# Kernel tuning notes

Measured on AMD Instinct MI355X. Metric: run time of the kernel, lower is better.

The kernel has to match this reference:

```python
import jax, jax.numpy as jnp
import numpy as np

K_NEIGHBORS = 8  # sparse_reads


def setup_inputs() -> dict:
    key = jax.random.key(0)
    k1, k2, k3, k4 = jax.random.split(key, 4)
    b, m, w, r, d_in = 32, 65536, 32, 4, 256
    xi = jax.random.normal(k1, (b, d_in), jnp.float32)
    sparse = jax.random.normal(k2, (b, m, w), jnp.float32)
    W_rk = jax.random.normal(k3, (r * w, d_in), jnp.float32) * 0.05  # read_keys_transform weight
    b_rk = jax.random.normal(k4, (r * w,), jnp.float32) * 0.01       # read_keys_transform bias
    return {"xi": xi, "sparse": sparse, "W_rk": W_rk, "b_rk": b_rk}


def reference(xi, sparse, W_rk, b_rk):
    b = xi.shape[0]
    m, w = sparse.shape[1], sparse.shape[2]
    r = W_rk.shape[0] // w
    # read keys: Linear(input_size, r*w) -> [b, r, w]
    read_keys = (xi @ W_rk.T + b_rk).reshape(b, r, w)
    # exact kNN replacing FLANN: squared L2 distances [b, r, m]
    d2 = (
        jnp.sum(read_keys * read_keys, -1)[..., None]
        - 2.0 * jnp.einsum('brw,bmw->brm', read_keys, sparse)
        + jnp.sum(sparse * sparse, -1)[:, None, :]
    )
    neg_d, idx = jax.lax.top_k(-d2, K_NEIGHBORS)  # K smallest distances
    dist = -neg_d                                  # [b, r, K]
    # gather the K nearest memory rows per (batch, head): [b, r, K, w]
    vecs = sparse[jnp.arange(b)[:, None, None], idx]
    # distances normalized by their max (per key), as in `distances / max(distances)`
    read_weights = dist / jnp.max(dist, -1, keepdims=True)
    # torch code stacks per-key over batch then over keys -> [r, b, K, w]
    read_vectors = jnp.transpose(vecs, (1, 0, 2, 3))
    read_weights = jnp.transpose(read_weights, (1, 0, 2))  # [r, b, K]
    return read_vectors, read_weights
```

## Files before the change

### kernel.cpp

```cpp
#include <hip/hip_runtime.h>

constexpr int Bb = 32;
constexpr int Mm = 65536;
constexpr int Ww = 32;
constexpr int Rr = 4;
constexpr int Dd = 256;
constexpr int Kk = 8;

constexpr int NB_A = 64;
constexpr int TPB_A = 256;
constexpr int ROWS_PER_BLOCK = Mm / NB_A;
constexpr int TILE_ROWS = 128;
constexpr int TILES = ROWS_PER_BLOCK / TILE_ROWS;
constexpr int NBUF = 3;
constexpr int CPL = NB_A * Kk / 64;

__device__ __forceinline__ void glds16(const float4* src, float4* dst_lds) {
  __builtin_amdgcn_global_load_lds(
      (const __attribute__((address_space(1))) void*)src,
      (__attribute__((address_space(3))) void*)dst_lds, 16, 0, 0);
}

__global__ __launch_bounds__(128) void rk_kernel(
    const float* __restrict__ xi, const float* __restrict__ Wrk,
    const float* __restrict__ brk, float* __restrict__ rk,
    float* __restrict__ rknorm) {
  const int b = blockIdx.x;
  const int tid = threadIdx.x;
  __shared__ float xs[Dd];
  __shared__ float rks[Rr * Ww];
  #pragma unroll
  for (int i = 0; i < Dd; i += 128) xs[i + tid] = xi[b * Dd + i + tid];
  __syncthreads();
  float acc = brk[tid];
  const float4* wr = reinterpret_cast<const float4*>(Wrk + (size_t)tid * Dd);
  #pragma unroll 4
  for (int i = 0; i < Dd / 4; ++i) {
    float4 wv = wr[i];
    acc = fmaf(wv.x, xs[4 * i + 0], acc);
    acc = fmaf(wv.y, xs[4 * i + 1], acc);
    acc = fmaf(wv.z, xs[4 * i + 2], acc);
    acc = fmaf(wv.w, xs[4 * i + 3], acc);
  }
  rk[b * Rr * Ww + tid] = acc;
  rks[tid] = acc;
  __syncthreads();
  if (tid < Rr) {
    float s = 0.f;
    #pragma unroll
    for (int j = 0; j < Ww; ++j) s = fmaf(rks[tid * Ww + j], rks[tid * Ww + j], s);
    rknorm[b * Rr + tid] = s;
  }
}

__global__ __launch_bounds__(TPB_A)
__attribute__((amdgpu_waves_per_eu(2, 3)))
void topk_partial(
    const float* __restrict__ sparse, const float* __restrict__ rk,
    const float* __restrict__ rknorm, float* __restrict__ cand_d,
    int* __restrict__ cand_i) {
  const int b = blockIdx.y;
  const int tid = threadIdx.x;
  const int lane = tid & 63;
  const int wid = tid >> 6;
  const float INF = __builtin_inff();

  __shared__ float4 rk4[Rr][8];
  __shared__ float rkn_s[Rr];
  __shared__ float4 tile[NBUF][TILE_ROWS * 8];

  const int rowBlk = blockIdx.x * ROWS_PER_BLOCK;
  const float4* sb4 =
      reinterpret_cast<const float4*>(sparse) + (size_t)b * Mm * 8;
  const int perm = ((lane >> 3) * 8) + ((lane & 7) ^ (lane >> 3));

  auto STAGE = [&](int buf, int t) {
    const float4* g0 = sb4 + (size_t)(rowBlk + t * TILE_ROWS + wid * 32) * 8;
    float4* l0 = &tile[buf][wid * 32 * 8];
    #pragma unroll
    for (int i = 0; i < 4; ++i) glds16(g0 + i * 64 + perm, l0 + i * 64);
  };

  STAGE(0, 0);
  STAGE(1, 1);

  if (tid < Rr * Ww) reinterpret_cast<float*>(rk4)[tid] = rk[b * Rr * Ww + tid];
  if (tid < Rr) rkn_s[tid] = rknorm[b * Rr + tid];
  __syncthreads();

  const int rowL = wid * 32 + (lane >> 1);
  const int rmask = rowL & 7;
  const int hsel = (tid & 1) * 4;

  float4 rkq[Rr][4];
  #pragma unroll
  for (int r = 0; r < Rr; ++r)
    #pragma unroll
    for (int j = 0; j < 4; ++j) rkq[r][j] = rk4[r][hsel + j];

  float d8[Rr][TILES];

  #pragma unroll
  for (int t = 0; t < TILES; ++t) {
    if (t + 2 < TILES) {
      asm volatile("s_waitcnt lgkmcnt(0)" ::: "memory");
      STAGE((t + 2) % NBUF, t + 2);
      asm volatile("s_waitcnt vmcnt(8)" ::: "memory");
    } else if (t + 1 < TILES) {
      asm volatile("s_waitcnt vmcnt(4)" ::: "memory");
    } else {
      asm volatile("s_waitcnt vmcnt(0)" ::: "memory");
    }
    const float4* tb = &tile[t % NBUF][rowL * 8];
    float a0 = 0.f, a1 = 0.f, a2 = 0.f, a3 = 0.f, ss = 0.f;
    #pragma unroll
    for (int j = 0; j < 4; ++j) {
      float4 v = tb[(hsel + j) ^ rmask];
      float4 k0 = rkq[0][j];
      float4 k1 = rkq[1][j];
      float4 k2 = rkq[2][j];
      float4 k3 = rkq[3][j];
      a0 = fmaf(k0.x, v.x, a0); a0 = fmaf(k0.y, v.y, a0);
      a0 = fmaf(k0.z, v.z, a0); a0 = fmaf(k0.w, v.w, a0);
      a1 = fmaf(k1.x, v.x, a1); a1 = fmaf(k1.y, v.y, a1);
      a1 = fmaf(k1.z, v.z, a1); a1 = fmaf(k1.w, v.w, a1);
      a2 = fmaf(k2.x, v.x, a2); a2 = fmaf(k2.y, v.y, a2);
      a2 = fmaf(k2.z, v.z, a2); a2 = fmaf(k2.w, v.w, a2);
      a3 = fmaf(k3.x, v.x, a3); a3 = fmaf(k3.y, v.y, a3);
      a3 = fmaf(k3.z, v.z, a3); a3 = fmaf(k3.w, v.w, a3);
      ss = fmaf(v.x, v.x, ss); ss = fmaf(v.y, v.y, ss);
      ss = fmaf(v.z, v.z, ss); ss = fmaf(v.w, v.w, ss);
    }
    float p0 = fmaf(-2.f, a0, ss);
    float p1 = fmaf(-2.f, a1, ss);
    float p2 = fmaf(-2.f, a2, ss);
    float p3 = fmaf(-2.f, a3, ss);
    p0 += __shfl_xor(p0, 1);
    p1 += __shfl_xor(p1, 1);
    p2 += __shfl_xor(p2, 1);
    p3 += __shfl_xor(p3, 1);
    d8[0][t] = p0;
    d8[1][t] = p1;
    d8[2][t] = p2;
    d8[3][t] = p3;
  }

  __syncthreads();
  float* dmp = reinterpret_cast<float*>(&tile[0][0]);
  if ((tid & 1) == 0) {
    const int e = tid >> 1;
    #pragma unroll
    for (int r = 0; r < Rr; ++r) {
      float4* p = reinterpret_cast<float4*>(&dmp[(r * 128 + e) * 8]);
      p[0] = make_float4(d8[r][0], d8[r][1], d8[r][2], d8[r][3]);
      p[1] = make_float4(d8[r][4], d8[r][5], d8[r][6], d8[r][7]);
    }
  }
  __syncthreads();

  {
    const int r = wid;
    const int e0 = 2 * lane;
    const float rknr = rkn_s[r];
    float v[2][TILES];
    #pragma unroll
    for (int q = 0; q < 2; ++q) {
      const float4* p =
          reinterpret_cast<const float4*>(&dmp[(r * 128 + e0 + q) * 8]);
      float4 lo = p[0], hi = p[1];
      v[q][0] = lo.x; v[q][1] = lo.y; v[q][2] = lo.z; v[q][3] = lo.w;
      v[q][4] = hi.x; v[q][5] = hi.y; v[q][6] = hi.z; v[q][7] = hi.w;
    }
    const int base = rowBlk + e0;
    size_t o = ((size_t)(b * Rr + r) * NB_A + blockIdx.x) * Kk;
    #pragma unroll
    for (int k = 0; k < Kk; ++k) {
      float lv = v[0][0];
      int lrow = base;
      #pragma unroll
      for (int q = 0; q < 2; ++q)
        #pragma unroll
        for (int s = 0; s < TILES; ++s) {
          if (q == 0 && s == 0) continue;
          int row = base + q + s * TILE_ROWS;
          if (v[q][s] < lv || (v[q][s] == lv && row < lrow)) {
            lv = v[q][s]; lrow = row;
          }
        }
      float bv = lv;
      int bi = lrow;
      #pragma unroll
      for (int off = 32; off; off >>= 1) {
        float ov = __shfl_xor(bv, off);
        int oi = __shfl_xor(bi, off);
        if (ov < bv || (ov == bv && oi < bi)) { bv = ov; bi = oi; }
      }
      if (lane == 0) { cand_d[o + k] = bv + rknr; cand_i[o + k] = bi; }
      #pragma unroll
      for (int q = 0; q < 2; ++q)
        #pragma unroll
        for (int s = 0; s < TILES; ++s) {
          bool clr = (v[q][s] == bv) && (base + q + s * TILE_ROWS == bi);
          v[q][s] = clr ? INF : v[q][s];
        }
    }
  }
}

__global__ __launch_bounds__(64) void topk_final(
    const float* __restrict__ sparse, const float* __restrict__ cand_d,
    const int* __restrict__ cand_i, float* __restrict__ out) {
  const int br = blockIdx.x;
  const int b = br >> 2;
  const int r = br & 3;
  const int lane = threadIdx.x;
  const float INF = __builtin_inff();

  float ld[CPL];
  int li[CPL];
  const float* cd = cand_d + (size_t)br * (NB_A * Kk);
  const int* ci = cand_i + (size_t)br * (NB_A * Kk);
  #pragma unroll
  for (int t = 0; t < CPL; ++t) {
    ld[t] = cd[t * 64 + lane];
    li[t] = ci[t * 64 + lane];
  }
  #pragma unroll
  for (int i = 0; i < CPL - 1; ++i)
    #pragma unroll
    for (int j = 0; j < CPL - 1 - i; ++j)
      if (ld[j + 1] < ld[j] || (ld[j + 1] == ld[j] && li[j + 1] < li[j])) {
        float td = ld[j]; ld[j] = ld[j + 1]; ld[j + 1] = td;
        int ti = li[j]; li[j] = li[j + 1]; li[j + 1] = ti;
      }

  __shared__ float s_td[Kk];
  __shared__ int s_ti[Kk];
  #pragma unroll
  for (int k = 0; k < Kk; ++k) {
    float v = ld[0];
    int id = li[0];
    #pragma unroll
    for (int off = 32; off; off >>= 1) {
      float ov = __shfl_xor(v, off);
      int oi = __shfl_xor(id, off);
      if (ov < v || (ov == v && oi < id)) { v = ov; id = oi; }
    }
    if (lane == 0) { s_td[k] = v; s_ti[k] = id; }
    if (li[0] == id) {
      #pragma unroll
      for (int j = 0; j < CPL - 1; ++j) { ld[j] = ld[j + 1]; li[j] = li[j + 1]; }
      ld[CPL - 1] = INF;
      li[CPL - 1] = -1;
    }
  }
  __syncthreads();

  const float dmax = s_td[Kk - 1];
  if (lane < Kk)
    out[(size_t)Rr * Bb * Kk * Ww + ((size_t)r * Bb + b) * Kk + lane] =
        s_td[lane] / dmax;

  const float* sbase = sparse + (size_t)b * Mm * Ww;
  #pragma unroll
  for (int t = 0; t < (Kk * Ww) / 64; ++t) {
    int e = t * 64 + lane;
    int k = e >> 5;
    int j = e & 31;
    out[(((size_t)r * Bb + b) * Kk + k) * Ww + j] =
        sbase[(size_t)s_ti[k] * Ww + j];
  }
}

extern "C" void kernel_launch(void* const* d_in, const int* in_sizes, int n_in,
                              void* d_out, int out_size, void* d_ws,
                              size_t ws_size, hipStream_t stream) {
  const float* xi = (const float*)d_in[0];
  const float* sparse = (const float*)d_in[1];
  const float* Wrk = (const float*)d_in[2];
  const float* brk = (const float*)d_in[3];
  float* out = (float*)d_out;

  char* ws = (char*)d_ws;
  float* rk = (float*)ws;
  float* rknorm = (float*)(ws + 16384);
  float* cand_d = (float*)(ws + 16896);
  int* cand_i = (int*)(ws + 16896 + 262144);

  rk_kernel<<<Bb, 128, 0, stream>>>(xi, Wrk, brk, rk, rknorm);
  dim3 gridA(NB_A, Bb);
  topk_partial<<<gridA, TPB_A, 0, stream>>>(sparse, rk, rknorm, cand_d, cand_i);
  topk_final<<<Bb * Rr, 64, 0, stream>>>(sparse, cand_d, cand_i, out);
}
```

Before: 99.96 us.

## Split topk_partial across twice as many blocks with 4-lane rows and deeper prefetch

Doubles the number of row blocks per batch and halves the tile height, so each row is now handled by 4 lanes instead of 2 and the LDS pipeline is deepened to 4 buffers with 3 tiles in flight. The goal is higher occupancy (waves_per_eu 4) and more memory-level parallelism for the streaming pass over the sparse memory, which is bandwidth bound. The per-block top-k selection is simplified to one value per tile per lane. The cost is twice as many candidates for topk_final to merge and an extra shuffle per row, and the workspace offset for cand_i moves to match.

```diff
diff --git a/kernel.cpp b/kernel.cpp
--- a/kernel.cpp
+++ b/kernel.cpp
@@ -7,12 +7,12 @@
 constexpr int Dd = 256;
 constexpr int Kk = 8;
 
-constexpr int NB_A = 64;
+constexpr int NB_A = 128;
 constexpr int TPB_A = 256;
 constexpr int ROWS_PER_BLOCK = Mm / NB_A;
-constexpr int TILE_ROWS = 128;
+constexpr int TILE_ROWS = 64;
 constexpr int TILES = ROWS_PER_BLOCK / TILE_ROWS;
-constexpr int NBUF = 3;
+constexpr int NBUF = 4;
 constexpr int CPL = NB_A * Kk / 64;
 
 __device__ __forceinline__ void glds16(const float4* src, float4* dst_lds) {
@@ -54,7 +54,7 @@
 }
 
 __global__ __launch_bounds__(TPB_A)
-__attribute__((amdgpu_waves_per_eu(2, 3)))
+__attribute__((amdgpu_waves_per_eu(4)))
 void topk_partial(
     const float* __restrict__ sparse, const float* __restrict__ rk,
     const float* __restrict__ rknorm, float* __restrict__ cand_d,
@@ -69,53 +69,56 @@
   __shared__ float rkn_s[Rr];
   __shared__ float4 tile[NBUF][TILE_ROWS * 8];
 
+  if (tid < Rr * Ww) reinterpret_cast<float*>(rk4)[tid] = rk[b * Rr * Ww + tid];
+  if (tid < Rr) rkn_s[tid] = rknorm[b * Rr + tid];
+  __syncthreads();
+
   const int rowBlk = blockIdx.x * ROWS_PER_BLOCK;
   const float4* sb4 =
       reinterpret_cast<const float4*>(sparse) + (size_t)b * Mm * 8;
   const int perm = ((lane >> 3) * 8) + ((lane & 7) ^ (lane >> 3));
 
+  const int rowL = wid * 16 + (lane >> 2);
+  const int rmask = rowL & 7;
+  const int c0 = 2 * (lane & 3);
+
+  float4 rkq[Rr][2];
+  #pragma unroll
+  for (int r = 0; r < Rr; ++r) {
+    rkq[r][0] = rk4[r][c0];
+    rkq[r][1] = rk4[r][c0 + 1];
+  }
+
+  float d8[Rr][TILES];
+
   auto STAGE = [&](int buf, int t) {
-    const float4* g0 = sb4 + (size_t)(rowBlk + t * TILE_ROWS + wid * 32) * 8;
-    float4* l0 = &tile[buf][wid * 32 * 8];
-    #pragma unroll
-    for (int i = 0; i < 4; ++i) glds16(g0 + i * 64 + perm, l0 + i * 64);
+    const float4* g0 = sb4 + (size_t)(rowBlk + t * TILE_ROWS + wid * 16) * 8;
+    float4* l0 = &tile[buf][wid * 16 * 8];
+    #pragma unroll
+    for (int i = 0; i < 2; ++i) glds16(g0 + i * 64 + perm, l0 + i * 64);
   };
 
   STAGE(0, 0);
   STAGE(1, 1);
-
-  if (tid < Rr * Ww) reinterpret_cast<float*>(rk4)[tid] = rk[b * Rr * Ww + tid];
-  if (tid < Rr) rkn_s[tid] = rknorm[b * Rr + tid];
-  __syncthreads();
-
-  const int rowL = wid * 32 + (lane >> 1);
-  const int rmask = rowL & 7;
-  const int hsel = (tid & 1) * 4;
-
-  float4 rkq[Rr][4];
-  #pragma unroll
-  for (int r = 0; r < Rr; ++r)
-    #pragma unroll
-    for (int j = 0; j < 4; ++j) rkq[r][j] = rk4[r][hsel + j];
-
-  float d8[Rr][TILES];
-
+  STAGE(2, 2);
   #pragma unroll
   for (int t = 0; t < TILES; ++t) {
-    if (t + 2 < TILES) {
+    if (t + 3 < TILES) {
       asm volatile("s_waitcnt lgkmcnt(0)" ::: "memory");
-      STAGE((t + 2) % NBUF, t + 2);
-      asm volatile("s_waitcnt vmcnt(8)" ::: "memory");
+      STAGE((t + 3) % NBUF, t + 3);
+      asm volatile("s_waitcnt vmcnt(6)" ::: "memory");
+    } else if (t + 2 < TILES) {
+      asm volatile("s_waitcnt vmcnt(4)" ::: "memory");
     } else if (t + 1 < TILES) {
-      asm volatile("s_waitcnt vmcnt(4)" ::: "memory");
+      asm volatile("s_waitcnt vmcnt(2)" ::: "memory");
     } else {
       asm volatile("s_waitcnt vmcnt(0)" ::: "memory");
     }
     const float4* tb = &tile[t % NBUF][rowL * 8];
     float a0 = 0.f, a1 = 0.f, a2 = 0.f, a3 = 0.f, ss = 0.f;
     #pragma unroll
-    for (int j = 0; j < 4; ++j) {
-      float4 v = tb[(hsel + j) ^ rmask];
+    for (int j = 0; j < 2; ++j) {
+      float4 v = tb[(c0 + j) ^ rmask];
       float4 k0 = rkq[0][j];
       float4 k1 = rkq[1][j];
       float4 k2 = rkq[2][j];
@@ -135,10 +138,10 @@
     float p1 = fmaf(-2.f, a1, ss);
     float p2 = fmaf(-2.f, a2, ss);
     float p3 = fmaf(-2.f, a3, ss);
-    p0 += __shfl_xor(p0, 1);
-    p1 += __shfl_xor(p1, 1);
-    p2 += __shfl_xor(p2, 1);
-    p3 += __shfl_xor(p3, 1);
+    p0 += __shfl_xor(p0, 1); p0 += __shfl_xor(p0, 2);
+    p1 += __shfl_xor(p1, 1); p1 += __shfl_xor(p1, 2);
+    p2 += __shfl_xor(p2, 1); p2 += __shfl_xor(p2, 2);
+    p3 += __shfl_xor(p3, 1); p3 += __shfl_xor(p3, 2);
     d8[0][t] = p0;
     d8[1][t] = p1;
     d8[2][t] = p2;
@@ -147,46 +150,31 @@
 
   __syncthreads();
   float* dmp = reinterpret_cast<float*>(&tile[0][0]);
-  if ((tid & 1) == 0) {
-    const int e = tid >> 1;
-    #pragma unroll
-    for (int r = 0; r < Rr; ++r) {
-      float4* p = reinterpret_cast<float4*>(&dmp[(r * 128 + e) * 8]);
-      p[0] = make_float4(d8[r][0], d8[r][1], d8[r][2], d8[r][3]);
-      p[1] = make_float4(d8[r][4], d8[r][5], d8[r][6], d8[r][7]);
-    }
+  if ((lane & 3) == 0) {
+    #pragma unroll
+    for (int r = 0; r < Rr; ++r)
+      #pragma unroll
+      for (int t = 0; t < TILES; ++t)
+        dmp[r * ROWS_PER_BLOCK + t * TILE_ROWS + rowL] = d8[r][t];
   }
   __syncthreads();
 
   {
     const int r = wid;
-    const int e0 = 2 * lane;
     const float rknr = rkn_s[r];
-    float v[2][TILES];
-    #pragma unroll
-    for (int q = 0; q < 2; ++q) {
-      const float4* p =
-          reinterpret_cast<const float4*>(&dmp[(r * 128 + e0 + q) * 8]);
-      float4 lo = p[0], hi = p[1];
-      v[q][0] = lo.x; v[q][1] = lo.y; v[q][2] = lo.z; v[q][3] = lo.w;
-      v[q][4] = hi.x; v[q][5] = hi.y; v[q][6] = hi.z; v[q][7] = hi.w;
-    }
-    const int base = rowBlk + e0;
+    float v[TILES];
+    #pragma unroll
+    for (int i = 0; i < TILES; ++i)
+      v[i] = dmp[r * ROWS_PER_BLOCK + i * TILE_ROWS + lane];
+    const int base = rowBlk + lane;
     size_t o = ((size_t)(b * Rr + r) * NB_A + blockIdx.x) * Kk;
     #pragma unroll
     for (int k = 0; k < Kk; ++k) {
-      float lv = v[0][0];
+      float lv = v[0];
       int lrow = base;
       #pragma unroll
-      for (int q = 0; q < 2; ++q)
-        #pragma unroll
-        for (int s = 0; s < TILES; ++s) {
-          if (q == 0 && s == 0) continue;
-          int row = base + q + s * TILE_ROWS;
-          if (v[q][s] < lv || (v[q][s] == lv && row < lrow)) {
-            lv = v[q][s]; lrow = row;
-          }
-        }
+      for (int i = 1; i < TILES; ++i)
+        if (v[i] < lv) { lv = v[i]; lrow = base + i * TILE_ROWS; }
       float bv = lv;
       int bi = lrow;
       #pragma unroll
@@ -197,12 +185,10 @@
       }
       if (lane == 0) { cand_d[o + k] = bv + rknr; cand_i[o + k] = bi; }
       #pragma unroll
-      for (int q = 0; q < 2; ++q)
-        #pragma unroll
-        for (int s = 0; s < TILES; ++s) {
-          bool clr = (v[q][s] == bv) && (base + q + s * TILE_ROWS == bi);
-          v[q][s] = clr ? INF : v[q][s];
-        }
+      for (int i = 0; i < TILES; ++i) {
+        bool clr = (v[i] == bv) && (base + i * TILE_ROWS == bi);
+        v[i] = clr ? INF : v[i];
+      }
     }
   }
 }
@@ -285,7 +271,7 @@
   float* rk = (float*)ws;
   float* rknorm = (float*)(ws + 16384);
   float* cand_d = (float*)(ws + 16896);
-  int* cand_i = (int*)(ws + 16896 + 262144);
+  int* cand_i = (int*)(ws + 16896 + 524288);
 
   rk_kernel<<<Bb, 128, 0, stream>>>(xi, Wrk, brk, rk, rknorm);
   dim3 gridA(NB_A, Bb);
```

After: 122.8 us. 22.8% more time.
